# Performance work log

Hardware: AMD Instinct MI355X
Metric: run time of the kernel (lower is better)

Reference implementation:

```python
import jax, jax.numpy as jnp
import numpy as np

B, S, D, H = 4, 2048, 512, 8
HD = D // H  # 64


def setup_inputs() -> dict:
    key = jax.random.key(0)
    ks = jax.random.split(key, 7)
    scale = 1.0 / np.sqrt(D)
    return {
        "query": jax.random.normal(ks[0], (B, S, D), jnp.float32),
        "key": jax.random.normal(ks[1], (B, S, D), jnp.float32),
        "value": jax.random.normal(ks[2], (B, S, D), jnp.float32),
        # Only the `query` Linear and fc_out are actually used in the original forward
        "Wq": jax.random.uniform(ks[3], (D, D), jnp.float32, -scale, scale),
        "bq": jnp.zeros((D,), jnp.float32),
        "Wo": jax.random.uniform(ks[4], (D, D), jnp.float32, -scale, scale),
        "bo": jnp.zeros((D,), jnp.float32),
    }


def reference(query, key, value, Wq, bq, Wo, bo):
    # Faithful to source: Q, K, V all use the *query* projection (bug preserved)
    def proj(x):
        # [B,S,D] -> [B,H,S,HD]
        y = x @ Wq + bq
        return y.reshape(B, S, H, HD).transpose(0, 2, 1, 3)

    Q, K, V = proj(query), proj(key), proj(value)
    scores = jnp.einsum("bhqd,bhkd->bhqk", Q, K) / jnp.sqrt(jnp.float32(HD))
    attn = jax.nn.softmax(scores, axis=-1)
    x = jnp.einsum("bhqk,bhkd->bhqd", attn, V)
    x = x.transpose(0, 2, 1, 3).reshape(B, S, D)
    return x @ Wo + bo
```

## Files before the change

### kernel.cpp

```cpp
#include <hip/hip_runtime.h>
#include <math.h>

#define B_ 4
#define S_ 2048
#define D_ 512
#define H_ 8
#define HD_ 64
#define SZ_ (B_ * S_ * D_)
#define WSZ_ (D_ * D_)

#define QSCALE_ 0.18033688011112042f

typedef _Float16 v4h __attribute__((ext_vector_type(4)));
typedef _Float16 v8h __attribute__((ext_vector_type(8)));
typedef float    v4f __attribute__((ext_vector_type(4)));

__global__ __launch_bounds__(256) void cast_f16_kernel(const float* __restrict__ q,
                                                       const float* __restrict__ k,
                                                       const float* __restrict__ v,
                                                       _Float16* __restrict__ dst) {
    const float* src = (blockIdx.z == 0) ? q : ((blockIdx.z == 1) ? k : v);
    _Float16* d = dst + (size_t)blockIdx.z * SZ_;
    size_t off = ((size_t)blockIdx.x * 256 + threadIdx.x) * 8;
    float4 a = *(const float4*)&src[off];
    float4 b = *(const float4*)&src[off + 4];
    v8h p;
    p[0] = (_Float16)a.x; p[1] = (_Float16)a.y; p[2] = (_Float16)a.z; p[3] = (_Float16)a.w;
    p[4] = (_Float16)b.x; p[5] = (_Float16)b.y; p[6] = (_Float16)b.z; p[7] = (_Float16)b.w;
    *(v8h*)&d[off] = p;
}

__global__ __launch_bounds__(256) void wtrans_kernel(const float* __restrict__ Wq,
                                                     const float* __restrict__ Wo,
                                                     _Float16* __restrict__ Wt) {
    __shared__ float Ts[64][65];
    const float* W = blockIdx.z ? Wo : Wq;
    _Float16* dst = Wt + (size_t)blockIdx.z * WSZ_;
    const int t = threadIdx.x;
    const int k0 = blockIdx.y * 64, n0 = blockIdx.x * 64;
#pragma unroll
    for (int i = 0; i < 4; i++) {
        int c = t + i * 256;
        int kk = c >> 4, nc = (c & 15) * 4;
        float4 w = *(const float4*)&W[(size_t)(k0 + kk) * 512 + n0 + nc];
        Ts[nc + 0][kk] = w.x;
        Ts[nc + 1][kk] = w.y;
        Ts[nc + 2][kk] = w.z;
        Ts[nc + 3][kk] = w.w;
    }
    __syncthreads();
#pragma unroll
    for (int i = 0; i < 2; i++) {
        int c = t + i * 256;
        int n = c >> 3, kc = (c & 7) * 8;
        v8h p;
#pragma unroll
        for (int j = 0; j < 8; j++) p[j] = (_Float16)Ts[n][kc + j];
        *(v8h*)&dst[(size_t)(n0 + n) * 512 + k0 + kc] = p;
    }
}

__device__ __forceinline__ void mfma_gemm128(const _Float16* __restrict__ A,
                                             const _Float16* __restrict__ Bt,
                                             int m0, int n0, v4f (&acc)[4][4]) {
    __shared__ _Float16 As[128 * 40];
    __shared__ _Float16 Bs[128 * 40];
    const int t    = threadIdx.x;
    const int lane = t & 63;
    const int w    = t >> 6;
    const int wm   = w >> 1, wn = w & 1;
    const int quad = lane >> 4, l16 = lane & 15;

#pragma unroll
    for (int mi = 0; mi < 4; mi++)
#pragma unroll
        for (int ni = 0; ni < 4; ni++) acc[mi][ni] = (v4f)0.f;

    const int r0 = t >> 2, r1 = (t + 256) >> 2;
    const int kc0 = (t & 3) * 8;

    for (int k0 = 0; k0 < 512; k0 += 32) {
        v8h a0 = *(const v8h*)&A[(size_t)(m0 + r0) * 512 + k0 + kc0];
        v8h a1 = *(const v8h*)&A[(size_t)(m0 + r1) * 512 + k0 + kc0];
        v8h b0 = *(const v8h*)&Bt[(size_t)(n0 + r0) * 512 + k0 + kc0];
        v8h b1 = *(const v8h*)&Bt[(size_t)(n0 + r1) * 512 + k0 + kc0];
        __syncthreads();
        *(v8h*)&As[r0 * 40 + kc0] = a0;
        *(v8h*)&As[r1 * 40 + kc0] = a1;
        *(v8h*)&Bs[r0 * 40 + kc0] = b0;
        *(v8h*)&Bs[r1 * 40 + kc0] = b1;
        __syncthreads();

        v8h af[4], bf[4];
#pragma unroll
        for (int mi = 0; mi < 4; mi++)
            af[mi] = *(const v8h*)&As[(wm * 64 + mi * 16 + l16) * 40 + quad * 8];
#pragma unroll
        for (int ni = 0; ni < 4; ni++)
            bf[ni] = *(const v8h*)&Bs[(wn * 64 + ni * 16 + l16) * 40 + quad * 8];
#pragma unroll
        for (int mi = 0; mi < 4; mi++)
#pragma unroll
            for (int ni = 0; ni < 4; ni++)
                acc[mi][ni] = __builtin_amdgcn_mfma_f32_16x16x32_f16(af[mi], bf[ni], acc[mi][ni], 0, 0, 0);
    }
}

__global__ __launch_bounds__(256) void proj_mfma(const _Float16* __restrict__ Xh,
                                                 const _Float16* __restrict__ Wt,
                                                 const float* __restrict__ bq,
                                                 _Float16* __restrict__ Qh,
                                                 _Float16* __restrict__ Kh,
                                                 _Float16* __restrict__ VT) {
    const int z  = blockIdx.z;
    const int n0 = blockIdx.x * 128, m0 = blockIdx.y * 128;
    const int lane = threadIdx.x & 63, w = threadIdx.x >> 6;
    const int wm = w >> 1, wn = w & 1;
    const int quad = lane >> 4, l16 = lane & 15;

    v4f acc[4][4];
    mfma_gemm128(Xh + (size_t)z * SZ_, Wt, m0, n0, acc);

    if (z < 2) {
        _Float16* Y = z ? Kh : Qh;
        const float sc = z ? 1.f : QSCALE_;
#pragma unroll
        for (int mi = 0; mi < 4; mi++) {
            int mb = m0 + wm * 64 + mi * 16 + quad * 4;
#pragma unroll
            for (int ni = 0; ni < 4; ni++) {
                int n = n0 + wn * 64 + ni * 16 + l16;
                float bj = bq[n];
#pragma unroll
                for (int r = 0; r < 4; r++)
                    Y[(size_t)(mb + r) * 512 + n] = (_Float16)((acc[mi][ni][r] + bj) * sc);
            }
        }
    } else {
#pragma unroll
        for (int mi = 0; mi < 4; mi++) {
            int tile0 = (m0 & 2047) + wm * 64;
            int pos = tile0 + (mi >> 1) * 32 + quad * 8 + (mi & 1) * 4;
            int b = m0 >> 11;
#pragma unroll
            for (int ni = 0; ni < 4; ni++) {
                int n = n0 + wn * 64 + ni * 16 + l16;
                int h = n >> 6, d = n & 63;
                float bj = bq[n];
                v4h pk;
#pragma unroll
                for (int r = 0; r < 4; r++) pk[r] = (_Float16)(acc[mi][ni][r] + bj);
                *(v4h*)&VT[(((size_t)b * H_ + h) * HD_ + d) * S_ + pos] = pk;
            }
        }
    }
}

__global__ __launch_bounds__(256) void outproj_mfma(const _Float16* __restrict__ Xa,
                                                    const _Float16* __restrict__ Wt,
                                                    const float* __restrict__ bo,
                                                    float* __restrict__ out) {
    const int n0 = blockIdx.x * 128, m0 = blockIdx.y * 128;
    const int lane = threadIdx.x & 63, w = threadIdx.x >> 6;
    const int wm = w >> 1, wn = w & 1;
    const int quad = lane >> 4, l16 = lane & 15;

    v4f acc[4][4];
    mfma_gemm128(Xa, Wt + (size_t)WSZ_, m0, n0, acc);

#pragma unroll
    for (int mi = 0; mi < 4; mi++) {
        int mb = m0 + wm * 64 + mi * 16 + quad * 4;
#pragma unroll
        for (int ni = 0; ni < 4; ni++) {
            int n = n0 + wn * 64 + ni * 16 + l16;
            float bj = bo[n];
#pragma unroll
            for (int r = 0; r < 4; r++)
                out[(size_t)(mb + r) * 512 + n] = acc[mi][ni][r] + bj;
        }
    }
}

__global__ __launch_bounds__(256) void flash_attn_f16(const _Float16* __restrict__ Qh,
                                                      const _Float16* __restrict__ Kh,
                                                      const _Float16* __restrict__ VT,
                                                      _Float16* __restrict__ Xa) {
    __shared__ _Float16 Ks[128 * 72];
    __shared__ _Float16 Vs[64 * 136];

    const int t    = threadIdx.x;
    const int lane = t & 63;
    const int w    = t >> 6;
    const int quad = lane >> 4;
    const int l16  = lane & 15;
    const int q0   = blockIdx.x * 128;
    const int h    = blockIdx.y;
    const int b    = blockIdx.z;

    const size_t base  = (size_t)b * S_ * D_ + (size_t)h * HD_;
    const size_t vbase = ((size_t)b * H_ + h) * HD_ * (size_t)S_;

    v8h qf[2][2];
#pragma unroll
    for (int nb = 0; nb < 2; nb++) {
        const _Float16* qrow = Qh + base + (size_t)(q0 + w * 32 + nb * 16 + l16) * D_;
        qf[nb][0] = *(const v8h*)(qrow + quad * 8);
        qf[nb][1] = *(const v8h*)(qrow + 32 + quad * 8);
    }

    v4f o[2][4];
#pragma unroll
    for (int nb = 0; nb < 2; nb++)
#pragma unroll
        for (int i = 0; i < 4; i++) o[nb][i] = (v4f)0.f;
    float l_i[2] = {0.f, 0.f};

    for (int kk0 = 0; kk0 < S_; kk0 += 128) {
        v8h kv[4], vv[4];
#pragma unroll
        for (int i = 0; i < 4; i++) {
            int c = t + i * 256;
            int krow = c >> 3, kcf = c & 7;
            kv[i] = *(const v8h*)(Kh + base + (size_t)(kk0 + krow) * D_ + kcf * 8);
            int vd = c >> 4, vpc = c & 15;
            vv[i] = *(const v8h*)(VT + vbase + (size_t)vd * S_ + kk0 + vpc * 8);
        }
        __syncthreads();
#pragma unroll
        for (int i = 0; i < 4; i++) {
            int c = t + i * 256;
            int krow = c >> 3, kcf = c & 7;
            *(v8h*)&Ks[krow * 72 + kcf * 8] = kv[i];
            int vd = c >> 4, vpc = c & 15;
            *(v8h*)&Vs[vd * 136 + vpc * 8] = vv[i];
        }
        __syncthreads();

#pragma unroll
        for (int hh = 0; hh < 2; hh++) {
            v4f sc[4][2];
#pragma unroll
            for (int mb = 0; mb < 4; mb++)
#pragma unroll
                for (int nb = 0; nb < 2; nb++) sc[mb][nb] = (v4f)0.f;
#pragma unroll
            for (int ks = 0; ks < 2; ks++) {
#pragma unroll
                for (int mb = 0; mb < 4; mb++) {
                    v8h ak = *(const v8h*)&Ks[(hh * 64 + mb * 16 + l16) * 72 + ks * 32 + quad * 8];
#pragma unroll
                    for (int nb = 0; nb < 2; nb++)
                        sc[mb][nb] = __builtin_amdgcn_mfma_f32_16x16x32_f16(ak, qf[nb][ks], sc[mb][nb], 0, 0, 0);
                }
            }

            v4h pf[4][2];
#pragma unroll
            for (int nb = 0; nb < 2; nb++) {
                float rs = 0.f;
#pragma unroll
                for (int mb = 0; mb < 4; mb++)
#pragma unroll
                    for (int r = 0; r < 4; r++) {
                        float p = exp2f(sc[mb][nb][r]);
                        pf[mb][nb][r] = (_Float16)p;
                        rs += p;
                    }
                rs += __shfl_xor(rs, 16);
                rs += __shfl_xor(rs, 32);
                l_i[nb] += rs;
            }

#pragma unroll
            for (int p = 0; p < 2; p++) {
#pragma unroll
                for (int dblk = 0; dblk < 4; dblk++) {
                    v8h vf2 = *(const v8h*)&Vs[(dblk * 16 + l16) * 136 + hh * 64 + p * 32 + quad * 8];
                    v4h vlo = __builtin_shufflevector(vf2, vf2, 0, 1, 2, 3);
                    v4h vhi = __builtin_shufflevector(vf2, vf2, 4, 5, 6, 7);
#pragma unroll
                    for (int nb = 0; nb < 2; nb++) {
                        o[nb][dblk] = __builtin_amdgcn_mfma_f32_16x16x16f16(vlo, pf[2 * p][nb], o[nb][dblk], 0, 0, 0);
                        o[nb][dblk] = __builtin_amdgcn_mfma_f32_16x16x16f16(vhi, pf[2 * p + 1][nb], o[nb][dblk], 0, 0, 0);
                    }
                }
            }
        }
    }

#pragma unroll
    for (int nb = 0; nb < 2; nb++) {
        const float linv = 1.f / l_i[nb];
        const size_t rbase = base + (size_t)(q0 + w * 32 + nb * 16 + l16) * D_;
#pragma unroll
        for (int dblk = 0; dblk < 4; dblk++) {
            v4h st;
#pragma unroll
            for (int r = 0; r < 4; r++) st[r] = (_Float16)(o[nb][dblk][r] * linv);
            *(v4h*)&Xa[rbase + dblk * 16 + quad * 4] = st;
        }
    }
}

extern "C" void kernel_launch(void* const* d_in, const int* in_sizes, int n_in,
                              void* d_out, int out_size, void* d_ws, size_t ws_size,
                              hipStream_t stream) {
    const float* query = (const float*)d_in[0];
    const float* key   = (const float*)d_in[1];
    const float* value = (const float*)d_in[2];
    const float* Wq    = (const float*)d_in[3];
    const float* bq    = (const float*)d_in[4];
    const float* Wo    = (const float*)d_in[5];
    const float* bo    = (const float*)d_in[6];
    float* out = (float*)d_out;

    _Float16* ws = (_Float16*)d_ws;
    _Float16* Xh = ws;
    _Float16* Qh = ws + 3 * (size_t)SZ_;
    _Float16* Kh = ws + 4 * (size_t)SZ_;
    _Float16* VT = ws + 5 * (size_t)SZ_;
    _Float16* Xa = ws + 6 * (size_t)SZ_;
    _Float16* Wt = ws + 7 * (size_t)SZ_;

    cast_f16_kernel<<<dim3(SZ_ / 2048, 1, 3), 256, 0, stream>>>(query, key, value, Xh);
    wtrans_kernel<<<dim3(8, 8, 2), 256, 0, stream>>>(Wq, Wo, Wt);
    proj_mfma<<<dim3(4, 64, 3), 256, 0, stream>>>(Xh, Wt, bq, Qh, Kh, VT);
    flash_attn_f16<<<dim3(S_ / 128, H_, B_), 256, 0, stream>>>(Qh, Kh, VT, Xa);
    outproj_mfma<<<dim3(4, 64, 1), 256, 0, stream>>>(Xa, Wt, bo, out);
}
```

Measured before the change: 216.7 us.

## Split attention over key dimension and add combine kernel

Splits the flash-attention key loop into two halves run by separate blocks, doubling the grid from 512 to 1024 blocks. Each split writes unnormalized fp32 partial outputs and row sums, and a new combine kernel adds the two partials, normalizes, and casts to fp16. The softmax row-sum reduction is also moved out of the inner loop, so shuffles happen once at the end. The cost is extra fp32 traffic for the partial outputs and one more kernel launch, plus a workspace layout that reuses the Xh region.

```diff
diff --git a/kernel.cpp b/kernel.cpp
--- a/kernel.cpp
+++ b/kernel.cpp
@@ -185,18 +185,20 @@
 __global__ __launch_bounds__(256) void flash_attn_f16(const _Float16* __restrict__ Qh,
                                                       const _Float16* __restrict__ Kh,
                                                       const _Float16* __restrict__ VT,
-                                                      _Float16* __restrict__ Xa) {
+                                                      float* __restrict__ Op,
+                                                      float* __restrict__ lp) {
     __shared__ _Float16 Ks[128 * 72];
     __shared__ _Float16 Vs[64 * 136];
 
-    const int t    = threadIdx.x;
-    const int lane = t & 63;
-    const int w    = t >> 6;
-    const int quad = lane >> 4;
-    const int l16  = lane & 15;
-    const int q0   = blockIdx.x * 128;
-    const int h    = blockIdx.y;
-    const int b    = blockIdx.z;
+    const int t     = threadIdx.x;
+    const int lane  = t & 63;
+    const int w     = t >> 6;
+    const int quad  = lane >> 4;
+    const int l16   = lane & 15;
+    const int q0    = blockIdx.x * 128;
+    const int h     = blockIdx.y;
+    const int b     = blockIdx.z >> 1;
+    const int split = blockIdx.z & 1;
 
     const size_t base  = (size_t)b * S_ * D_ + (size_t)h * HD_;
     const size_t vbase = ((size_t)b * H_ + h) * HD_ * (size_t)S_;
@@ -214,9 +216,10 @@
     for (int nb = 0; nb < 2; nb++)
 #pragma unroll
         for (int i = 0; i < 4; i++) o[nb][i] = (v4f)0.f;
-    float l_i[2] = {0.f, 0.f};
-
-    for (int kk0 = 0; kk0 < S_; kk0 += 128) {
+    float l_lane[2] = {0.f, 0.f};
+
+    const int kbeg = split * (S_ / 2);
+    for (int kk0 = kbeg; kk0 < kbeg + S_ / 2; kk0 += 128) {
         v8h kv[4], vv[4];
 #pragma unroll
         for (int i = 0; i < 4; i++) {
@@ -258,18 +261,14 @@
             v4h pf[4][2];
 #pragma unroll
             for (int nb = 0; nb < 2; nb++) {
-                float rs = 0.f;
-#pragma unroll
-                for (int mb = 0; mb < 4; mb++)
-#pragma unroll
-                    for (int r = 0; r < 4; r++) {
-                        float p = exp2f(sc[mb][nb][r]);
-                        pf[mb][nb][r] = (_Float16)p;
-                        rs += p;
-                    }
-                rs += __shfl_xor(rs, 16);
-                rs += __shfl_xor(rs, 32);
-                l_i[nb] += rs;
+#pragma unroll
+                for (int mb = 0; mb < 4; mb++) {
+                    v4f pv;
+#pragma unroll
+                    for (int r = 0; r < 4; r++) pv[r] = exp2f(sc[mb][nb][r]);
+                    pf[mb][nb] = __builtin_convertvector(pv, v4h);
+                    l_lane[nb] += (pv[0] + pv[1]) + (pv[2] + pv[3]);
+                }
             }
 
 #pragma unroll
@@ -289,18 +288,42 @@
         }
     }
 
+    float* Ops = Op + (size_t)split * SZ_;
 #pragma unroll
     for (int nb = 0; nb < 2; nb++) {
-        const float linv = 1.f / l_i[nb];
-        const size_t rbase = base + (size_t)(q0 + w * 32 + nb * 16 + l16) * D_;
-#pragma unroll
-        for (int dblk = 0; dblk < 4; dblk++) {
-            v4h st;
-#pragma unroll
-            for (int r = 0; r < 4; r++) st[r] = (_Float16)(o[nb][dblk][r] * linv);
-            *(v4h*)&Xa[rbase + dblk * 16 + quad * 4] = st;
-        }
-    }
+        float rs = l_lane[nb];
+        rs += __shfl_xor(rs, 16);
+        rs += __shfl_xor(rs, 32);
+        int qrow = q0 + w * 32 + nb * 16 + l16;
+        if (quad == 0)
+            lp[(size_t)split * (B_ * S_ * H_) + ((size_t)b * S_ + qrow) * H_ + h] = rs;
+        const size_t rbase = base + (size_t)qrow * D_;
+#pragma unroll
+        for (int dblk = 0; dblk < 4; dblk++)
+            *(v4f*)&Ops[rbase + dblk * 16 + quad * 4] = o[nb][dblk];
+    }
+}
+
+__global__ __launch_bounds__(256) void combine_kernel(const float* __restrict__ Op,
+                                                      const float* __restrict__ lp,
+                                                      _Float16* __restrict__ Xa) {
+    size_t idx = ((size_t)blockIdx.x * 256 + threadIdx.x) * 8;
+    int row = (int)(idx >> 9);
+    int h   = (int)((idx >> 6) & 7);
+    float l1 = lp[(size_t)row * H_ + h];
+    float l2 = lp[(size_t)(B_ * S_ * H_) + (size_t)row * H_ + h];
+    float linv = 1.f / (l1 + l2);
+    v4f a0 = *(const v4f*)&Op[idx];
+    v4f a1 = *(const v4f*)&Op[idx + 4];
+    v4f b0 = *(const v4f*)&Op[SZ_ + idx];
+    v4f b1 = *(const v4f*)&Op[SZ_ + idx + 4];
+    v8h r;
+#pragma unroll
+    for (int j = 0; j < 4; j++) {
+        r[j]     = (_Float16)((a0[j] + b0[j]) * linv);
+        r[j + 4] = (_Float16)((a1[j] + b1[j]) * linv);
+    }
+    *(v8h*)&Xa[idx] = r;
 }
 
 extern "C" void kernel_launch(void* const* d_in, const int* in_sizes, int n_in,
@@ -316,16 +339,19 @@
     float* out = (float*)d_out;
 
     _Float16* ws = (_Float16*)d_ws;
-    _Float16* Xh = ws;
-    _Float16* Qh = ws + 3 * (size_t)SZ_;
-    _Float16* Kh = ws + 4 * (size_t)SZ_;
-    _Float16* VT = ws + 5 * (size_t)SZ_;
-    _Float16* Xa = ws + 6 * (size_t)SZ_;
-    _Float16* Wt = ws + 7 * (size_t)SZ_;
+    _Float16* Qh = ws;
+    _Float16* Kh = ws + (size_t)SZ_;
+    _Float16* VT = ws + 2 * (size_t)SZ_;
+    _Float16* Xa = ws + 3 * (size_t)SZ_;
+    _Float16* Wt = ws + 4 * (size_t)SZ_;
+    _Float16* Xh = ws + 4 * (size_t)SZ_ + SZ_ / 8;
+    float*    Op = (float*)Xh;
+    float*    lp = (float*)(Xh + 8 * (size_t)SZ_);
 
     cast_f16_kernel<<<dim3(SZ_ / 2048, 1, 3), 256, 0, stream>>>(query, key, value, Xh);
     wtrans_kernel<<<dim3(8, 8, 2), 256, 0, stream>>>(Wq, Wo, Wt);
     proj_mfma<<<dim3(4, 64, 3), 256, 0, stream>>>(Xh, Wt, bq, Qh, Kh, VT);
-    flash_attn_f16<<<dim3(S_ / 128, H_, B_), 256, 0, stream>>>(Qh, Kh, VT, Xa);
+    flash_attn_f16<<<dim3(S_ / 128, H_, B_ * 2), 256, 0, stream>>>(Qh, Kh, VT, Op, lp);
+    combine_kernel<<<dim3(SZ_ / 2048), 256, 0, stream>>>(Op, lp, Xa);
     outproj_mfma<<<dim3(4, 64, 1), 256, 0, stream>>>(Xa, Wt, bo, out);
 }
```

Measured after the change: 215.9 us. Within noise of the previous version (-0.4%).
